# Kernel tuning notes

Measured on AMD Instinct MI355X. Metric: run time of the kernel, lower is better.

Reference implementation:

```python
import jax, jax.numpy as jnp
import numpy as np
import math

NEG_INF = -1e9  # keras Softmax masking uses a large negative additive constant

def setup_inputs() -> dict:
    key = jax.random.key(0)
    k1, k2, k3, k4 = jax.random.split(key, 4)
    B, T, C, H = 4, 4096, 1024, 128
    x = jax.random.normal(k1, (B, T, C), dtype=jnp.float32)
    Wq = jax.random.normal(k2, (C, H), dtype=jnp.float32) * (1.0 / math.sqrt(C))
    Wk = jax.random.normal(k3, (C, H), dtype=jnp.float32) * (1.0 / math.sqrt(C))
    Wv = jax.random.normal(k4, (C, H), dtype=jnp.float32) * (1.0 / math.sqrt(C))
    return {"x": x, "Wq": Wq, "Wk": Wk, "Wv": Wv}

def reference(x, Wq, Wk, Wv):
    # x: [B, T, C]; projections are bias-free Dense layers
    B, T, C = x.shape
    q = jnp.einsum('btc,ch->bth', x, Wq)  # [B, T, H]
    k = jnp.einsum('btc,ch->bth', x, Wk)  # [B, T, H]
    v = jnp.einsum('btc,ch->bth', x, Wv)  # [B, T, H]
    # NOTE: original scales by sqrt(C) (the input channel dim), not sqrt(head_size)
    wei = jnp.einsum('bth,bsh->bts', q, k) / math.sqrt(C)  # [B, T, T]
    causal = jnp.tril(jnp.ones((T, T), dtype=bool))
    wei = jnp.where(causal[None, :, :], wei, NEG_INF)
    wei = jax.nn.softmax(wei, axis=-1)
    # dropout is identity at inference
    out = jnp.einsum('bts,bsh->bth', wei, v)  # [B, T, H]
    return out
```

## Files before the change

kernel.cpp:

```cpp
#include <hip/hip_runtime.h>
#include <hip/hip_bf16.h>

typedef __bf16 bf16x8 __attribute__((ext_vector_type(8)));
typedef __bf16 bf16x4 __attribute__((ext_vector_type(4)));
typedef float  f32x4  __attribute__((ext_vector_type(4)));

#define NB 4
#define TT 4096
#define CC 1024
#define HH 128
#define PS 72
#define MNEG -30000.0f

__device__ inline void gload16(const void* g, void* l) {
  __builtin_amdgcn_global_load_lds(
      (const __attribute__((address_space(1))) void*)g,
      (__attribute__((address_space(3))) void*)l, 16, 0, 0);
}

__global__ void detect_dtype(const unsigned int* __restrict__ xw, int* __restrict__ flag) {
  int t = threadIdx.x;
  int cnt = 0;
#pragma unroll
  for (int i = 0; i < 4; ++i) {
    unsigned int w = xw[t + 64 * i];
    int e = (int)((w >> 7) & 0xFFu);
    cnt += (e >= 100 && e <= 135) ? 1 : 0;
  }
  cnt += __shfl_xor(cnt, 1);  cnt += __shfl_xor(cnt, 2);  cnt += __shfl_xor(cnt, 4);
  cnt += __shfl_xor(cnt, 8);  cnt += __shfl_xor(cnt, 16); cnt += __shfl_xor(cnt, 32);
  if (t == 0) *flag = (cnt >= 128) ? 1 : 0;
}

__global__ __launch_bounds__(256) void transpose_w3(
    const void* __restrict__ Wq, const void* __restrict__ Wk,
    const void* __restrict__ Wv, __bf16* __restrict__ Wt,
    const int* __restrict__ flagp) {
  int isbf = *flagp;
  int which = blockIdx.y;
  const void* W = (which == 0) ? Wq : (which == 1) ? Wk : Wv;
  int idx = blockIdx.x * 256 + threadIdx.x;
  int h = idx >> 10, c = idx & 1023;
  __bf16 val;
  if (isbf) val = ((const __bf16*)W)[c * HH + h];
  else      val = (__bf16)(((const float*)W)[c * HH + h]);
  size_t o = (size_t)(c >> 6) * 24576 + (size_t)which * 8192 +
             (size_t)((c >> 3) & 7) * 1024 + (size_t)h * 8 + (c & 7);
  Wt[o] = val;
}

__global__ __launch_bounds__(768) void qkv_proj(
    const void* __restrict__ x, const __bf16* __restrict__ Wt,
    __bf16* __restrict__ q, __bf16* __restrict__ ktl, __bf16* __restrict__ vtl,
    const int* __restrict__ flagp) {
  __shared__ __align__(16) __bf16 XT[2][4096];
  __shared__ __align__(16) __bf16 WTs[2][24576];
  int isbf = *flagp;
  int tid = threadIdx.x, lane = tid & 63, wave = tid >> 6;
  int which = wave >> 2, rowgrp = wave & 3;
  int l16 = lane & 15, quad = lane >> 4;
  int row0 = blockIdx.x * 64;
  f32x4 acc[8] = {};

#define STAGE(ss, b)                                                          \
  for (int i = wave; i < 56; i += 12) {                                       \
    if (i < 8) {                                                              \
      int row = i * 8 + (lane >> 3), g = lane & 7;                            \
      bf16x8 pk;                                                              \
      if (isbf) {                                                             \
        pk = *(const bf16x8*)((const __bf16*)x + (size_t)(row0 + row) * CC +  \
                              (ss) * 64 + g * 8);                             \
      } else {                                                                \
        const float* xf = (const float*)x + (size_t)(row0 + row) * CC +       \
                          (ss) * 64 + g * 8;                                  \
        f32x4 lo = *(const f32x4*)xf;                                         \
        f32x4 hi = *(const f32x4*)(xf + 4);                                   \
        for (int j = 0; j < 4; ++j) { pk[j] = (__bf16)lo[j]; pk[j+4] = (__bf16)hi[j]; } \
      }                                                                       \
      *(bf16x8*)(&XT[b][g * 512 + (row ^ g) * 8]) = pk;                       \
    } else {                                                                  \
      int j = i - 8;                                                          \
      gload16(Wt + (size_t)(ss) * 24576 + j * 512 + lane * 8,                 \
              &WTs[b][j * 512]);                                              \
    }                                                                         \
  }

  STAGE(0, 0);
  for (int s = 0; s < 16; ++s) {
    int cb = s & 1;
    __syncthreads();
    if (s + 1 < 16) { STAGE(s + 1, cb ^ 1); }
#pragma unroll
    for (int t = 0; t < 2; ++t) {
      int g = t * 4 + quad;
      bf16x8 a = *(const bf16x8*)(&XT[cb][g * 512 + ((rowgrp * 16 + l16) ^ g) * 8]);
#pragma unroll
      for (int nt = 0; nt < 8; ++nt) {
        bf16x8 b = *(const bf16x8*)(&WTs[cb][(size_t)which * 8192 + g * 1024 + (nt * 16 + l16) * 8]);
        acc[nt] = __builtin_amdgcn_mfma_f32_16x16x32_bf16(a, b, acc[nt], 0, 0, 0);
      }
    }
  }
#undef STAGE

  int tile = row0 >> 6;
  if (which == 0) {
#pragma unroll
    for (int nt = 0; nt < 8; ++nt)
#pragma unroll
      for (int r = 0; r < 4; ++r) {
        int row = row0 + rowgrp * 16 + quad * 4 + r;
        q[(size_t)row * HH + nt * 16 + l16] = (__bf16)acc[nt][r];
      }
  } else if (which == 1) {
    __bf16* kb = ktl + (size_t)tile * 8192;
#pragma unroll
    for (int nt = 0; nt < 8; ++nt) {
      int h = nt * 16 + l16, g = h >> 3, j = h & 7;
#pragma unroll
      for (int r = 0; r < 4; ++r) {
        int sidx = rowgrp * 16 + quad * 4 + r;
        kb[g * 512 + sidx * 8 + j] = (__bf16)acc[nt][r];
      }
    }
  } else {
    __bf16* vb = vtl + (size_t)tile * 8192;
#pragma unroll
    for (int nt = 0; nt < 8; ++nt) {
      int h = nt * 16 + l16;
      int sb = rowgrp * 16 + quad * 4;
      bf16x4 pk;
#pragma unroll
      for (int r = 0; r < 4; ++r) pk[r] = (__bf16)acc[nt][r];
      *(bf16x4*)(vb + (sb >> 3) * 1024 + h * 8 + (sb & 7)) = pk;
    }
  }
}

__global__ __launch_bounds__(768, 3) void flash_attn(
    const __bf16* __restrict__ q, const __bf16* __restrict__ ktl,
    const __bf16* __restrict__ vtl, void* __restrict__ out,
    const int* __restrict__ flagp) {
  __shared__ __align__(16) __bf16 PL[12][16 * PS];
  __shared__ float CMB[2][64][132];
  __shared__ float CL[2][64];

  int bx = blockIdx.x;
  int qt = bx & 63;
  int batch = bx >> 6;

  int tid = threadIdx.x, lane = tid & 63, wave = tid >> 6;
  int kg = wave >> 2, rowgrp = wave & 3;
  int l16 = lane & 15, quad = lane >> 4;
  int qb = qt * 64;
  const __bf16* qp  = q   + (size_t)batch * TT * HH;
  const __bf16* ktb = ktl + (size_t)batch * TT * HH;
  const __bf16* vtb = vtl + (size_t)batch * TT * HH;

  bf16x8 qf[4];
  {
    const __bf16* qrow = qp + (size_t)(qb + rowgrp * 16 + l16) * HH + quad * 8;
#pragma unroll
    for (int ks = 0; ks < 4; ++ks) qf[ks] = *(const bf16x8*)(qrow + ks * 32);
  }
  bf16x8 onesf;
#pragma unroll
  for (int j = 0; j < 8; ++j) onesf[j] = (l16 == 0) ? (__bf16)1.0f : (__bf16)0.0f;

  f32x4 acc_o[8] = {};
  f32x4 acc_l = {};
  const float SC = 0.0450842200278f;
  const float M0 = 4.0f;
  int qrl = qb + rowgrp * 16 + quad * 4;

  for (int jt = kg; jt <= qt; jt += 3) {
    const __bf16* kt  = ktb + (size_t)jt * 8192;
    const __bf16* vt2 = vtb + (size_t)jt * 8192;

    bf16x8 kf[4][4];
#pragma unroll
    for (int ks = 0; ks < 4; ++ks)
#pragma unroll
      for (int kn = 0; kn < 4; ++kn)
        kf[ks][kn] = *(const bf16x8*)(kt + ((4 * ks + quad) * 64 + kn * 16 + l16) * 8);

    f32x4 accs[4] = {};
#pragma unroll
    for (int ks = 0; ks < 4; ++ks)
#pragma unroll
      for (int kn = 0; kn < 4; ++kn)
        accs[kn] = __builtin_amdgcn_mfma_f32_16x16x32_bf16(qf[ks], kf[ks][kn], accs[kn], 0, 0, 0);

    bf16x8 vf[2][8];
#pragma unroll
    for (int ks2 = 0; ks2 < 2; ++ks2)
#pragma unroll
      for (int nt = 0; nt < 8; ++nt)
        vf[ks2][nt] = *(const bf16x8*)(vt2 + (ks2 * 4 + quad) * 1024 + (nt * 16 + l16) * 8);

    float pv[4][4];
    if (jt == qt) {
#pragma unroll
      for (int nt = 0; nt < 4; ++nt) {
        int kcol = jt * 64 + nt * 16 + l16;
#pragma unroll
        for (int r = 0; r < 4; ++r) {
          float z = fmaf(accs[nt][r], SC, -M0);
          z = (kcol <= qrl + r) ? z : MNEG;
          pv[nt][r] = exp2f(z);
        }
      }
    } else {
#pragma unroll
      for (int nt = 0; nt < 4; ++nt)
#pragma unroll
        for (int r = 0; r < 4; ++r)
          pv[nt][r] = exp2f(fmaf(accs[nt][r], SC, -M0));
    }

    __bf16* pw = &PL[wave][0];
#pragma unroll
    for (int nt = 0; nt < 4; ++nt)
#pragma unroll
      for (int r = 0; r < 4; ++r)
        pw[(quad * 4 + r) * PS + nt * 16 + l16] = (__bf16)pv[nt][r];

#pragma unroll
    for (int ks2 = 0; ks2 < 2; ++ks2) {
      bf16x8 pa = *(const bf16x8*)(pw + l16 * PS + ks2 * 32 + quad * 8);
      acc_l = __builtin_amdgcn_mfma_f32_16x16x32_bf16(pa, onesf, acc_l, 0, 0, 0);
#pragma unroll
      for (int nt = 0; nt < 8; ++nt)
        acc_o[nt] = __builtin_amdgcn_mfma_f32_16x16x32_bf16(pa, vf[ks2][nt], acc_o[nt], 0, 0, 0);
    }
  }

  int qrow = rowgrp * 16 + quad * 4;
  if (kg > 0) {
#pragma unroll
    for (int nt = 0; nt < 8; ++nt)
#pragma unroll
      for (int r = 0; r < 4; ++r)
        CMB[kg - 1][qrow + r][nt * 16 + l16] = acc_o[nt][r];
    if (l16 == 0) {
#pragma unroll
      for (int r = 0; r < 4; ++r) CL[kg - 1][qrow + r] = acc_l[r];
    }
  }
  __syncthreads();
  if (kg == 0) {
    int isbf = *flagp;
    float inv[4];
#pragma unroll
    for (int r = 0; r < 4; ++r) {
      float lr = __shfl(acc_l[r], lane & 48);
      lr += CL[0][qrow + r] + CL[1][qrow + r];
      inv[r] = 1.f / fmaxf(lr, 1e-30f);
    }
    __bf16* ob = (__bf16*)out + (size_t)batch * TT * HH;
    float*  of = (float*)out  + (size_t)batch * TT * HH;
#pragma unroll
    for (int nt = 0; nt < 8; ++nt)
#pragma unroll
      for (int r = 0; r < 4; ++r) {
        int row = qb + qrow + r;
        int col = nt * 16 + l16;
        float val = acc_o[nt][r] + CMB[0][qrow + r][col] + CMB[1][qrow + r][col];
        val *= inv[r];
        size_t idx = (size_t)row * HH + col;
        if (isbf) ob[idx] = (__bf16)val;
        else      of[idx] = val;
      }
  }
}

extern "C" void kernel_launch(void* const* d_in, const int* in_sizes, int n_in,
                              void* d_out, int out_size, void* d_ws, size_t ws_size,
                              hipStream_t stream) {
  const void* x  = d_in[0];
  const void* Wq = d_in[1];
  const void* Wk = d_in[2];
  const void* Wv = d_in[3];
  char* wsb = (char*)d_ws;
  __bf16* q   = (__bf16*)wsb;
  __bf16* ktl = q   + (size_t)NB * TT * HH;
  __bf16* vtl = ktl + (size_t)NB * TT * HH;
  __bf16* wt  = vtl + (size_t)NB * TT * HH;
  size_t base = (((size_t)(3 * NB * TT * HH + 3 * CC * HH) * 2) + 255) & ~(size_t)255;
  int* flag = (int*)(wsb + base);
  (void)ws_size; (void)in_sizes; (void)n_in; (void)out_size;

  detect_dtype<<<1, 64, 0, stream>>>((const unsigned int*)x, flag);
  transpose_w3<<<dim3(512, 3), 256, 0, stream>>>(Wq, Wk, Wv, wt, flag);
  qkv_proj<<<256, 768, 0, stream>>>(x, wt, q, ktl, vtl, flag);
  flash_attn<<<NB * 64, 768, 0, stream>>>(q, ktl, vtl, d_out, flag);
}
```

Before: 190.6 us.

## Pair causal query tiles per block to balance attention work

```diff
diff --git a/kernel.cpp b/kernel.cpp
--- a/kernel.cpp
+++ b/kernel.cpp
@@ -40,7 +40,7 @@
   int which = blockIdx.y;
   const void* W = (which == 0) ? Wq : (which == 1) ? Wk : Wv;
   int idx = blockIdx.x * 256 + threadIdx.x;
-  int h = idx >> 10, c = idx & 1023;
+  int h = idx & 127, c = idx >> 7;
   __bf16 val;
   if (isbf) val = ((const __bf16*)W)[c * HH + h];
   else      val = (__bf16)(((const float*)W)[c * HH + h]);
@@ -142,24 +142,31 @@
     const __bf16* __restrict__ vtl, void* __restrict__ out,
     const int* __restrict__ flagp) {
   __shared__ __align__(16) __bf16 PL[12][16 * PS];
-  __shared__ float CMB[2][64][132];
-  __shared__ float CL[2][64];
+  __shared__ float CMB[4][32][132];
+  __shared__ float CL[4][32];
 
   int bx = blockIdx.x;
-  int qt = bx & 63;
-  int batch = bx >> 6;
+  int batch = bx >> 6, qt0 = bx & 63;
 
   int tid = threadIdx.x, lane = tid & 63, wave = tid >> 6;
-  int kg = wave >> 2, rowgrp = wave & 3;
+  int p = wave >> 1, rowgrp = wave & 1;
   int l16 = lane & 15, quad = lane >> 4;
-  int qb = qt * 64;
+
+  int kA = (6 * (qt0 + 1) + 32) / 65;
+  kA = max(1, min(5, kA));
+  int unit, kg, nkg, qtu, rh;
+  if (p < kA) { unit = 0; kg = p;      nkg = kA;     qtu = qt0;      rh = 0; }
+  else        { unit = 1; kg = p - kA; nkg = 6 - kA; qtu = 63 - qt0; rh = 1; }
+
+  int qb = qtu * 64;
+  int rb = rh * 32 + rowgrp * 16;
   const __bf16* qp  = q   + (size_t)batch * TT * HH;
   const __bf16* ktb = ktl + (size_t)batch * TT * HH;
   const __bf16* vtb = vtl + (size_t)batch * TT * HH;
 
   bf16x8 qf[4];
   {
-    const __bf16* qrow = qp + (size_t)(qb + rowgrp * 16 + l16) * HH + quad * 8;
+    const __bf16* qrow = qp + (size_t)(qb + rb + l16) * HH + quad * 8;
 #pragma unroll
     for (int ks = 0; ks < 4; ++ks) qf[ks] = *(const bf16x8*)(qrow + ks * 32);
   }
@@ -171,9 +178,9 @@
   f32x4 acc_l = {};
   const float SC = 0.0450842200278f;
   const float M0 = 4.0f;
-  int qrl = qb + rowgrp * 16 + quad * 4;
-
-  for (int jt = kg; jt <= qt; jt += 3) {
+  int qrl = qb + rb + quad * 4;
+
+  for (int jt = kg; jt <= qtu; jt += nkg) {
     const __bf16* kt  = ktb + (size_t)jt * 8192;
     const __bf16* vt2 = vtb + (size_t)jt * 8192;
 
@@ -199,7 +206,7 @@
         vf[ks2][nt] = *(const bf16x8*)(vt2 + (ks2 * 4 + quad) * 1024 + (nt * 16 + l16) * 8);
 
     float pv[4][4];
-    if (jt == qt) {
+    if (jt == qtu) {
 #pragma unroll
       for (int nt = 0; nt < 4; ++nt) {
         int kcol = jt * 64 + nt * 16 + l16;
@@ -235,37 +242,41 @@
     }
   }
 
-  int qrow = rowgrp * 16 + quad * 4;
+  int rr = rowgrp * 16 + quad * 4;
   if (kg > 0) {
+    int slot = (unit == 0) ? (kg - 1) : (kA - 1 + kg - 1);
 #pragma unroll
     for (int nt = 0; nt < 8; ++nt)
 #pragma unroll
       for (int r = 0; r < 4; ++r)
-        CMB[kg - 1][qrow + r][nt * 16 + l16] = acc_o[nt][r];
+        CMB[slot][rr + r][nt * 16 + l16] = acc_o[nt][r];
     if (l16 == 0) {
 #pragma unroll
-      for (int r = 0; r < 4; ++r) CL[kg - 1][qrow + r] = acc_l[r];
+      for (int r = 0; r < 4; ++r) CL[slot][rr + r] = acc_l[r];
     }
   }
   __syncthreads();
   if (kg == 0) {
+    int lo  = (unit == 0) ? 0 : kA - 1;
+    int cnt = (unit == 0) ? kA - 1 : 5 - kA;
     int isbf = *flagp;
+    __bf16* ob = (__bf16*)out + (size_t)batch * TT * HH;
+    float*  of = (float*)out  + (size_t)batch * TT * HH;
     float inv[4];
 #pragma unroll
     for (int r = 0; r < 4; ++r) {
       float lr = __shfl(acc_l[r], lane & 48);
-      lr += CL[0][qrow + r] + CL[1][qrow + r];
+      for (int c = 0; c < cnt; ++c) lr += CL[lo + c][rr + r];
       inv[r] = 1.f / fmaxf(lr, 1e-30f);
     }
-    __bf16* ob = (__bf16*)out + (size_t)batch * TT * HH;
-    float*  of = (float*)out  + (size_t)batch * TT * HH;
 #pragma unroll
     for (int nt = 0; nt < 8; ++nt)
 #pragma unroll
       for (int r = 0; r < 4; ++r) {
-        int row = qb + qrow + r;
+        int row = qb + rh * 32 + rr + r;
         int col = nt * 16 + l16;
-        float val = acc_o[nt][r] + CMB[0][qrow + r][col] + CMB[1][qrow + r][col];
+        float val = acc_o[nt][r];
+        for (int c = 0; c < cnt; ++c) val += CMB[lo + c][rr + r][col];
         val *= inv[r];
         size_t idx = (size_t)row * HH + col;
         if (isbf) ob[idx] = (__bf16)val;
```

New measurement: 181.5 us. 4.8% less time.
